# Kernel tuning notes

Measured on AMD Instinct MI355X. Metric: run time of the kernel, lower is better.

The kernel has to match this reference:

```python
import jax, jax.numpy as jnp
import numpy as np

EPS = 1e-5

def hardsigmoid(x):
    # torch F.hardsigmoid: clip(x/6 + 0.5, 0, 1)
    return jnp.clip(x / 6.0 + 0.5, 0.0, 1.0)

def setup_inputs() -> dict:
    T, B, D = 2048, 8, 1024
    key = jax.random.key(0)
    k1, k2 = jax.random.split(key)
    x = jax.random.normal(k1, (T, B, D), dtype=jnp.float32)
    c = jnp.zeros((B, D), dtype=jnp.float32)
    # params
    w_ufr = jax.random.normal(k2, (3 * D, D), dtype=jnp.float32) * (1.0 / np.sqrt(D))
    gamma = jnp.ones((D,), dtype=jnp.float32)
    beta = jnp.zeros((D,), dtype=jnp.float32)
    return {"x": x, "c": c, "w_ufr": w_ufr, "gamma": gamma, "beta": beta}

def reference(x, c, w_ufr, gamma, beta):
    residual = x
    # LayerNorm over last dim
    mu = jnp.mean(x, axis=-1, keepdims=True)
    var = jnp.mean(jnp.square(x - mu), axis=-1, keepdims=True)
    x_norm = (x - mu) * jax.lax.rsqrt(var + EPS) * gamma + beta
    # fused projection to u, f, r: (T,B,D) @ (D,3D)
    ufr = jnp.einsum('tbd,ed->tbe', x_norm, w_ufr)
    u, f, r = jnp.split(ufr, 3, axis=-1)
    f_gate = hardsigmoid(f)
    r_gate = hardsigmoid(r)
    # diagonal linear recurrence: c_t = f_t * c_{t-1} + (1 - f_t) * u_t
    def step(c_prev, inputs):
        ft, ut = inputs
        c_curr = ft * c_prev + (1.0 - ft) * ut
        return c_curr, c_curr
    c_last, c_all = jax.lax.scan(step, c, (f_gate, u))
    tanh_approx = c_all / (1.0 + jnp.abs(c_all))  # softsign
    hs = r_gate * tanh_approx + (1.0 - r_gate) * x_norm
    return (residual + hs, c_last)
```

## Files before the change

kernel.cpp:

```cpp
#include <hip/hip_runtime.h>
#include <stdint.h>


#define T_SEQ 2048
#define BATCH 8
#define DIM 1024
#define M_SZ (T_SEQ * BATCH)
#define N_SZ (3 * DIM)
#define K_SZ DIM
#define NCHUNK 32
#define CLEN (T_SEQ / NCHUNK)

#define BM 128
#define BN 128
#define BK 32

typedef __attribute__((ext_vector_type(8))) __bf16 bf16x8;
typedef __attribute__((ext_vector_type(4))) float f32x4;

__device__ __forceinline__ unsigned short f2bf(float f) {
  unsigned int u = __float_as_uint(f);
  u += 0x7FFFu + ((u >> 16) & 1u);
  return (unsigned short)(u >> 16);
}
__device__ __forceinline__ float bf2f(unsigned short s) {
  return __uint_as_float(((unsigned int)s) << 16);
}
__device__ __forceinline__ void gload16(const void* g, void* l) {
  __builtin_amdgcn_global_load_lds(
      (__attribute__((address_space(1))) void*)const_cast<void*>(g),
      (__attribute__((address_space(3))) void*)l, 16, 0, 0);
}

__global__ __launch_bounds__(256) void cvt_kernel(const float* __restrict__ w,
                                                  unsigned short* __restrict__ wb) {
  const int i = blockIdx.x * 256 + threadIdx.x;
  const float4 v = reinterpret_cast<const float4*>(w)[i];
  ushort4 o;
  o.x = f2bf(v.x); o.y = f2bf(v.y); o.z = f2bf(v.z); o.w = f2bf(v.w);
  reinterpret_cast<ushort4*>(wb)[i] = o;
}

__global__ __launch_bounds__(256) void ln_kernel(const float* __restrict__ x,
                                                 const float* __restrict__ gamma,
                                                 const float* __restrict__ beta,
                                                 unsigned short* __restrict__ xn) {
  const int row = blockIdx.x;
  const int tid = threadIdx.x;
  const float4 v = reinterpret_cast<const float4*>(x + (size_t)row * DIM)[tid];
  float s = v.x + v.y + v.z + v.w;
  float q = v.x * v.x + v.y * v.y + v.z * v.z + v.w * v.w;
#pragma unroll
  for (int off = 32; off > 0; off >>= 1) {
    s += __shfl_down(s, off);
    q += __shfl_down(q, off);
  }
  __shared__ float sbuf[8];
  const int wv = tid >> 6, ln = tid & 63;
  if (ln == 0) { sbuf[wv] = s; sbuf[4 + wv] = q; }
  __syncthreads();
  s = sbuf[0] + sbuf[1] + sbuf[2] + sbuf[3];
  q = sbuf[4] + sbuf[5] + sbuf[6] + sbuf[7];
  const float mu = s * (1.0f / DIM);
  const float rstd = rsqrtf(q * (1.0f / DIM) - mu * mu + 1e-5f);
  const float4 g = reinterpret_cast<const float4*>(gamma)[tid];
  const float4 b = reinterpret_cast<const float4*>(beta)[tid];
  ushort4 o;
  o.x = f2bf((v.x - mu) * rstd * g.x + b.x);
  o.y = f2bf((v.y - mu) * rstd * g.y + b.y);
  o.z = f2bf((v.z - mu) * rstd * g.z + b.z);
  o.w = f2bf((v.w - mu) * rstd * g.w + b.w);
  reinterpret_cast<ushort4*>(xn + (size_t)row * DIM)[tid] = o;
}

__global__ __launch_bounds__(256) void gemm_kernel(const unsigned short* __restrict__ A,
                                                   const unsigned short* __restrict__ W,
                                                   unsigned short* __restrict__ C) {
  __shared__ unsigned short smA[BM * BK];
  __shared__ unsigned short smB[BN * BK];
  const int tid = threadIdx.x;
  const int lane = tid & 63;
  const int wid = tid >> 6;
  const int wm = wid >> 1, wn = wid & 1;
  const int bm0 = blockIdx.y * BM, bn0 = blockIdx.x * BN;

  const int ldr = wid * 16 + (lane >> 2);
  const int ldc = (lane & 3) * 8;
  const unsigned short* gA0 = A + (size_t)(bm0 + ldr) * K_SZ + ldc;
  const unsigned short* gA1 = gA0 + (size_t)64 * K_SZ;
  const unsigned short* gB0 = W + (size_t)(bn0 + ldr) * K_SZ + ldc;
  const unsigned short* gB1 = gB0 + (size_t)64 * K_SZ;
  unsigned short* sA0 = &smA[(wid * 16) * BK];
  unsigned short* sA1 = &smA[(64 + wid * 16) * BK];
  unsigned short* sB0 = &smB[(wid * 16) * BK];
  unsigned short* sB1 = &smB[(64 + wid * 16) * BK];

  f32x4 acc[4][4] = {};
  const int fr = lane & 15;
  const int ko = (lane >> 4) * 8;

  for (int kt = 0; kt < K_SZ / BK; ++kt) {
    gload16(gA0, sA0);
    gload16(gA1, sA1);
    gload16(gB0, sB0);
    gload16(gB1, sB1);
    gA0 += BK; gA1 += BK; gB0 += BK; gB1 += BK;
    __syncthreads();
    bf16x8 af[4], bfr[4];
#pragma unroll
    for (int i = 0; i < 4; i++)
      af[i] = *(const bf16x8*)&smA[(wm * 64 + i * 16 + fr) * BK + ko];
#pragma unroll
    for (int j = 0; j < 4; j++)
      bfr[j] = *(const bf16x8*)&smB[(wn * 64 + j * 16 + fr) * BK + ko];
#pragma unroll
    for (int i = 0; i < 4; i++)
#pragma unroll
      for (int j = 0; j < 4; j++)
        acc[i][j] = __builtin_amdgcn_mfma_f32_16x16x32_bf16(af[i], bfr[j], acc[i][j], 0, 0, 0);
    __syncthreads();
  }

  const int gate = (bn0 >= DIM);
  const int fq = lane >> 4;
#pragma unroll
  for (int i = 0; i < 4; i++) {
#pragma unroll
    for (int j = 0; j < 4; j++) {
      const int col = bn0 + wn * 64 + j * 16 + fr;
      size_t base = (size_t)(bm0 + wm * 64 + i * 16 + fq * 4) * N_SZ + col;
#pragma unroll
      for (int r = 0; r < 4; r++) {
        float v = acc[i][j][r];
        if (gate) v = fminf(fmaxf(v * (1.0f / 6.0f) + 0.5f, 0.0f), 1.0f);
        C[base + (size_t)r * N_SZ] = f2bf(v);
      }
    }
  }
}

__global__ __launch_bounds__(256) void scan1_kernel(const unsigned short* __restrict__ ufr,
                                                    float* __restrict__ Ac,
                                                    float* __restrict__ Bc) {
  const int lin = blockIdx.x * 256 + threadIdx.x;
  const int d = lin & (DIM - 1);
  const int b = (lin >> 10) & (BATCH - 1);
  const int g = lin >> 13;
  const unsigned short* p = ufr + (size_t)(g * CLEN) * (BATCH * N_SZ) + (size_t)b * N_SZ + d;
  float Aa = 1.0f, Bb = 0.0f;
#pragma unroll 8
  for (int t = 0; t < CLEN; t++) {
    const float u = bf2f(p[0]);
    const float f = bf2f(p[DIM]);
    Aa *= f;
    Bb = f * Bb + (1.0f - f) * u;
    p += BATCH * N_SZ;
  }
  Ac[lin] = Aa;
  Bc[lin] = Bb;
}

__global__ __launch_bounds__(256) void scan2_kernel(const float* __restrict__ Ac,
                                                    const float* __restrict__ Bc,
                                                    const float* __restrict__ c0,
                                                    float* __restrict__ cstart,
                                                    float* __restrict__ clast) {
  const int lin = blockIdx.x * 256 + threadIdx.x;
  float c = c0[lin];
#pragma unroll
  for (int g = 0; g < NCHUNK; g++) {
    cstart[g * (BATCH * DIM) + lin] = c;
    c = Ac[g * (BATCH * DIM) + lin] * c + Bc[g * (BATCH * DIM) + lin];
  }
  clast[lin] = c;
}

__global__ __launch_bounds__(256) void scan3_kernel(const unsigned short* __restrict__ ufr,
                                                    const unsigned short* __restrict__ xn,
                                                    const float* __restrict__ x,
                                                    const float* __restrict__ cstart,
                                                    float* __restrict__ out) {
  const int lin = blockIdx.x * 256 + threadIdx.x;
  const int d = lin & (DIM - 1);
  const int b = (lin >> 10) & (BATCH - 1);
  const int g = lin >> 13;
  float c = cstart[g * (BATCH * DIM) + b * DIM + d];
  const unsigned short* p = ufr + (size_t)(g * CLEN) * (BATCH * N_SZ) + (size_t)b * N_SZ + d;
  size_t xo = (size_t)(g * CLEN) * (BATCH * DIM) + (size_t)b * DIM + d;
#pragma unroll 4
  for (int t = 0; t < CLEN; t++) {
    const float u = bf2f(p[0]);
    const float f = bf2f(p[DIM]);
    const float r = bf2f(p[2 * DIM]);
    c = f * c + (1.0f - f) * u;
    const float ts = c / (1.0f + fabsf(c));
    const float xv = bf2f(xn[xo]);
    out[xo] = x[xo] + r * ts + (1.0f - r) * xv;
    p += BATCH * N_SZ;
    xo += BATCH * DIM;
  }
}

extern "C" void kernel_launch(void* const* d_in, const int* in_sizes, int n_in,
                              void* d_out, int out_size, void* d_ws, size_t ws_size,
                              hipStream_t stream) {
  const float* x = (const float*)d_in[0];
  const float* c0 = (const float*)d_in[1];
  const float* w = (const float*)d_in[2];
  const float* gamma = (const float*)d_in[3];
  const float* beta = (const float*)d_in[4];
  float* out = (float*)d_out;
  float* clast = out + (size_t)M_SZ * DIM;

  char* ws = (char*)d_ws;
  unsigned short* xn = (unsigned short*)ws;
  unsigned short* ufr = (unsigned short*)(ws + 33554432ull);
  float* Ac = (float*)(ws + 134217728ull);
  float* Bc = (float*)(ws + 135266304ull);
  float* cst = (float*)(ws + 136314880ull);
  unsigned short* wb = (unsigned short*)(ws + 137363456ull);

  cvt_kernel<<<(N_SZ * K_SZ / 4) / 256, 256, 0, stream>>>(w, wb);
  ln_kernel<<<M_SZ, 256, 0, stream>>>(x, gamma, beta, xn);
  dim3 ggrid(N_SZ / BN, M_SZ / BM);
  gemm_kernel<<<ggrid, 256, 0, stream>>>(xn, wb, ufr);
  scan1_kernel<<<(NCHUNK * BATCH * DIM) / 256, 256, 0, stream>>>(ufr, Ac, Bc);
  scan2_kernel<<<(BATCH * DIM) / 256, 256, 0, stream>>>(Ac, Bc, c0, cst, clast);
  scan3_kernel<<<(NCHUNK * BATCH * DIM) / 256, 256, 0, stream>>>(ufr, xn, x, cst, out);
}
```

Baseline: 216.2 us.

## Enlarge GEMM tiles to 256x256 with 4-stage async LDS pipeline

```diff
diff --git a/kernel.cpp b/kernel.cpp
--- a/kernel.cpp
+++ b/kernel.cpp
@@ -11,9 +11,10 @@
 #define NCHUNK 32
 #define CLEN (T_SEQ / NCHUNK)
 
-#define BM 128
-#define BN 128
-#define BK 32
+#define GBM 256
+#define GBN 256
+#define GBK 32
+#define NKT (K_SZ / GBK)
 
 typedef __attribute__((ext_vector_type(8))) __bf16 bf16x8;
 typedef __attribute__((ext_vector_type(4))) float f32x4;
@@ -73,62 +74,84 @@
   reinterpret_cast<ushort4*>(xn + (size_t)row * DIM)[tid] = o;
 }
 
-__global__ __launch_bounds__(256) void gemm_kernel(const unsigned short* __restrict__ A,
+__global__ __launch_bounds__(512) void gemm_kernel(const unsigned short* __restrict__ A,
                                                    const unsigned short* __restrict__ W,
                                                    unsigned short* __restrict__ C) {
-  __shared__ unsigned short smA[BM * BK];
-  __shared__ unsigned short smB[BN * BK];
+  __shared__ unsigned short smem[2 * 4 * GBM * GBK];
   const int tid = threadIdx.x;
   const int lane = tid & 63;
   const int wid = tid >> 6;
-  const int wm = wid >> 1, wn = wid & 1;
-  const int bm0 = blockIdx.y * BM, bn0 = blockIdx.x * BN;
-
-  const int ldr = wid * 16 + (lane >> 2);
-  const int ldc = (lane & 3) * 8;
-  const unsigned short* gA0 = A + (size_t)(bm0 + ldr) * K_SZ + ldc;
-  const unsigned short* gA1 = gA0 + (size_t)64 * K_SZ;
-  const unsigned short* gB0 = W + (size_t)(bn0 + ldr) * K_SZ + ldc;
-  const unsigned short* gB1 = gB0 + (size_t)64 * K_SZ;
-  unsigned short* sA0 = &smA[(wid * 16) * BK];
-  unsigned short* sA1 = &smA[(64 + wid * 16) * BK];
-  unsigned short* sB0 = &smB[(wid * 16) * BK];
-  unsigned short* sB1 = &smB[(64 + wid * 16) * BK];
-
-  f32x4 acc[4][4] = {};
+  const int wm = wid >> 2, wn = wid & 3;
+  const int bm0 = blockIdx.y * GBM, bn0 = blockIdx.x * GBN;
+
+  const int stgRow = wid * 32 + (lane >> 2);
+  const int stgCol = (lane & 3) * 8;
+  const unsigned short* gA = A + (size_t)(bm0 + stgRow) * K_SZ + stgCol;
+  const unsigned short* gB = W + (size_t)(bn0 + stgRow) * K_SZ + stgCol;
+  unsigned short* sAb = smem + wid * 32 * GBK;
+  unsigned short* sBb = smem + 4 * GBM * GBK + wid * 32 * GBK;
+
+#define STAGE(bufi, t) do {                                        \
+    const size_t ko_ = (size_t)(t) * GBK;                          \
+    unsigned short* sa_ = sAb + (bufi) * (GBM * GBK);              \
+    unsigned short* sb_ = sBb + (bufi) * (GBN * GBK);              \
+    gload16(gA + ko_, sa_);                                        \
+    gload16(gA + ko_ + (size_t)16 * K_SZ, sa_ + 16 * GBK);         \
+    gload16(gB + ko_, sb_);                                        \
+    gload16(gB + ko_ + (size_t)16 * K_SZ, sb_ + 16 * GBK);         \
+  } while (0)
+
+  f32x4 acc[8][4] = {};
   const int fr = lane & 15;
-  const int ko = (lane >> 4) * 8;
-
-  for (int kt = 0; kt < K_SZ / BK; ++kt) {
-    gload16(gA0, sA0);
-    gload16(gA1, sA1);
-    gload16(gB0, sB0);
-    gload16(gB1, sB1);
-    gA0 += BK; gA1 += BK; gB0 += BK; gB1 += BK;
-    __syncthreads();
-    bf16x8 af[4], bfr[4];
-#pragma unroll
-    for (int i = 0; i < 4; i++)
-      af[i] = *(const bf16x8*)&smA[(wm * 64 + i * 16 + fr) * BK + ko];
+  const int ko8 = (lane >> 4) * 8;
+
+  STAGE(0, 0);
+  STAGE(1, 1);
+  STAGE(2, 2);
+  asm volatile("s_waitcnt vmcnt(8)" ::: "memory");
+  __builtin_amdgcn_s_barrier();
+  asm volatile("" ::: "memory");
+
+  for (int kt = 0; kt < NKT; ++kt) {
+    const int cur = kt & 3;
+    if (kt < NKT - 3) STAGE((kt + 3) & 3, kt + 3);
+
+    const unsigned short* sa = smem + cur * (GBM * GBK);
+    const unsigned short* sb = smem + 4 * GBM * GBK + cur * (GBN * GBK);
+    bf16x8 af[8], bf[4];
+#pragma unroll
+    for (int i = 0; i < 8; i++)
+      af[i] = *(const bf16x8*)&sa[(wm * 128 + i * 16 + fr) * GBK + ko8];
 #pragma unroll
     for (int j = 0; j < 4; j++)
-      bfr[j] = *(const bf16x8*)&smB[(wn * 64 + j * 16 + fr) * BK + ko];
-#pragma unroll
-    for (int i = 0; i < 4; i++)
+      bf[j] = *(const bf16x8*)&sb[(wn * 64 + j * 16 + fr) * GBK + ko8];
+
+    __builtin_amdgcn_s_setprio(1);
+#pragma unroll
+    for (int i = 0; i < 8; i++)
 #pragma unroll
       for (int j = 0; j < 4; j++)
-        acc[i][j] = __builtin_amdgcn_mfma_f32_16x16x32_bf16(af[i], bfr[j], acc[i][j], 0, 0, 0);
-    __syncthreads();
-  }
+        acc[i][j] = __builtin_amdgcn_mfma_f32_16x16x32_bf16(af[i], bf[j], acc[i][j], 0, 0, 0);
+    __builtin_amdgcn_s_setprio(0);
+
+    if (kt < NKT - 3)       asm volatile("s_waitcnt vmcnt(8)" ::: "memory");
+    else if (kt == NKT - 3) asm volatile("s_waitcnt vmcnt(4)" ::: "memory");
+    else if (kt == NKT - 2) asm volatile("s_waitcnt vmcnt(0)" ::: "memory");
+    if (kt < NKT - 1) {
+      __builtin_amdgcn_s_barrier();
+      asm volatile("" ::: "memory");
+    }
+  }
+#undef STAGE
 
   const int gate = (bn0 >= DIM);
   const int fq = lane >> 4;
 #pragma unroll
-  for (int i = 0; i < 4; i++) {
+  for (int i = 0; i < 8; i++) {
 #pragma unroll
     for (int j = 0; j < 4; j++) {
       const int col = bn0 + wn * 64 + j * 16 + fr;
-      size_t base = (size_t)(bm0 + wm * 64 + i * 16 + fq * 4) * N_SZ + col;
+      size_t base = (size_t)(bm0 + wm * 128 + i * 16 + fq * 4) * N_SZ + col;
 #pragma unroll
       for (int r = 0; r < 4; r++) {
         float v = acc[i][j][r];
@@ -222,8 +245,8 @@
 
   cvt_kernel<<<(N_SZ * K_SZ / 4) / 256, 256, 0, stream>>>(w, wb);
   ln_kernel<<<M_SZ, 256, 0, stream>>>(x, gamma, beta, xn);
-  dim3 ggrid(N_SZ / BN, M_SZ / BM);
-  gemm_kernel<<<ggrid, 256, 0, stream>>>(xn, wb, ufr);
+  dim3 ggrid(N_SZ / GBN, M_SZ / GBM);
+  gemm_kernel<<<ggrid, 512, 0, stream>>>(xn, wb, ufr);
   scan1_kernel<<<(NCHUNK * BATCH * DIM) / 256, 256, 0, stream>>>(ufr, Ac, Bc);
   scan2_kernel<<<(BATCH * DIM) / 256, 256, 0, stream>>>(Ac, Bc, c0, cst, clast);
   scan3_kernel<<<(NCHUNK * BATCH * DIM) / 256, 256, 0, stream>>>(ufr, xn, x, cst, out);
```

After: 210.7 us. -2.5%, faster.
